# Optimization experiments

Hardware: AMD Instinct MI355X
Metric: run time of the kernel (lower is better)

The kernel has to match this reference:

```python
import jax, jax.numpy as jnp
import numpy as np

N, D = 2097152, 10  # tokens, feature dim (pinned by nn.Linear(10,10))


def setup_inputs() -> dict:
    key = jax.random.key(0)
    kx, kr, kw1, kb1, kw2, kb2 = jax.random.split(key, 6)
    s = 1.0 / np.sqrt(D)  # torch nn.Linear default init range
    x = jax.random.normal(kx, (N, D), dtype=jnp.float32)
    route = jax.random.randint(kr, (N,), 0, 2, dtype=jnp.int32)  # RandScatter decision
    W1 = jax.random.uniform(kw1, (D, D), jnp.float32, -s, s)
    b1 = jax.random.uniform(kb1, (D,), jnp.float32, -s, s)
    W2 = jax.random.uniform(kw2, (D, D), jnp.float32, -s, s)
    b2 = jax.random.uniform(kb2, (D,), jnp.float32, -s, s)
    return {"x": x, "W1": W1, "b1": b1, "W2": W2, "b2": b2, "route": route}


def reference(x, W1, b1, W2, b2, route):
    # Original: scatter rows by `route` to expert1/expert2 (Linear 10->10),
    # then gather back to original row order. Equivalent dense form:
    # out[i] = expert_{route[i]}(x[i]). The 10x10 GEMMs are negligible, so
    # computing both branches and selecting is the efficient vectorized form.
    y0 = x @ W1.T + b1  # [N, D] expert1 on all rows
    y1 = x @ W2.T + b2  # [N, D] expert2 on all rows
    return jnp.where((route == 0)[:, None], y0, y1)
```

## Files before the change

### kernel.cpp

```cpp
#include <hip/hip_runtime.h>


#define ROWS_PER_THREAD 4
#define BLOCK 256
#define D 10

__global__ __launch_bounds__(BLOCK) void moe_kernel(
    const float* __restrict__ x,
    const float* __restrict__ W1,
    const float* __restrict__ b1,
    const float* __restrict__ W2,
    const float* __restrict__ b2,
    const int*   __restrict__ route,
    float*       __restrict__ out,
    int n)
{
    const long long tid  = (long long)blockIdx.x * BLOCK + threadIdx.x;
    const long long row0 = tid * ROWS_PER_THREAD;
    if (row0 >= n) return;

    if (row0 + ROWS_PER_THREAD <= n) {
        const float4* __restrict__ xv = (const float4*)(x + row0 * D);
        float4*       __restrict__ ov = (float4*)(out + row0 * D);

        float v[ROWS_PER_THREAD * D];
        #pragma unroll
        for (int i = 0; i < 10; ++i) {
            float4 t = xv[i];
            v[i * 4 + 0] = t.x; v[i * 4 + 1] = t.y;
            v[i * 4 + 2] = t.z; v[i * 4 + 3] = t.w;
        }

        int4 rt = *(const int4*)(route + row0);
        int rsel[ROWS_PER_THREAD] = {rt.x, rt.y, rt.z, rt.w};

        #pragma unroll
        for (int r = 0; r < ROWS_PER_THREAD; ++r) {
            float y[D];
            #pragma unroll
            for (int j = 0; j < D; ++j) {
                float y0 = b1[j];
                float y1 = b2[j];
                #pragma unroll
                for (int k = 0; k < D; ++k) {
                    const float xk = v[r * D + k];
                    y0 = fmaf(xk, W1[j * D + k], y0);
                    y1 = fmaf(xk, W2[j * D + k], y1);
                }
                y[j] = (rsel[r] != 0) ? y1 : y0;
            }
            #pragma unroll
            for (int j = 0; j < D; ++j) v[r * D + j] = y[j];
        }

        #pragma unroll
        for (int i = 0; i < 10; ++i) {
            float4 t;
            t.x = v[i * 4 + 0]; t.y = v[i * 4 + 1];
            t.z = v[i * 4 + 2]; t.w = v[i * 4 + 3];
            ov[i] = t;
        }
    } else {
        for (long long row = row0; row < n; ++row) {
            const int sel = route[row];
            for (int j = 0; j < D; ++j) {
                float y0 = b1[j];
                float y1 = b2[j];
                for (int k = 0; k < D; ++k) {
                    const float xk = x[row * D + k];
                    y0 = fmaf(xk, W1[j * D + k], y0);
                    y1 = fmaf(xk, W2[j * D + k], y1);
                }
                out[row * D + j] = sel ? y1 : y0;
            }
        }
    }
}

extern "C" void kernel_launch(void* const* d_in, const int* in_sizes, int n_in,
                              void* d_out, int out_size, void* d_ws, size_t ws_size,
                              hipStream_t stream) {
    const float* x     = (const float*)d_in[0];
    const float* W1    = (const float*)d_in[1];
    const float* b1    = (const float*)d_in[2];
    const float* W2    = (const float*)d_in[3];
    const float* b2    = (const float*)d_in[4];
    const int*   route = (const int*)d_in[5];
    float*       out   = (float*)d_out;

    const int n = in_sizes[5];
    const int rows_per_block = BLOCK * ROWS_PER_THREAD;
    const int blocks = (n + rows_per_block - 1) / rows_per_block;

    moe_kernel<<<blocks, BLOCK, 0, stream>>>(x, W1, b1, W2, b2, route, out, n);
}
```

Before: 179.8 us.

## Stage rows through LDS per wave for fully coalesced global loads and stores

Each wave now loads a contiguous 128-row chunk of x with lane-strided float4 loads into shared memory, then each lane reads its own 2 rows back from LDS. Outputs are written into LDS and stored back with coalesced lane-strided float4 stores. Rows per thread drop from 4 to 2, which raises the thread count and lowers register pressure. The cost of the layout transpose is extra LDS traffic, possible bank conflicts from the stride-5 float4 access, and wave-level barriers.

```diff
diff --git a/kernel.cpp b/kernel.cpp
--- a/kernel.cpp
+++ b/kernel.cpp
@@ -1,9 +1,11 @@
 #include <hip/hip_runtime.h>
 
 
-#define ROWS_PER_THREAD 4
 #define BLOCK 256
 #define D 10
+#define ROWS_PER_WAVE 128
+#define ROWS_PER_BLOCK 512
+#define F4_PER_WAVE 320
 
 __global__ __launch_bounds__(BLOCK) void moe_kernel(
     const float* __restrict__ x,
@@ -15,63 +17,85 @@
     float*       __restrict__ out,
     int n)
 {
-    const long long tid  = (long long)blockIdx.x * BLOCK + threadIdx.x;
-    const long long row0 = tid * ROWS_PER_THREAD;
-    if (row0 >= n) return;
+    __shared__ float4 lds[(BLOCK / 64) * F4_PER_WAVE];
 
-    if (row0 + ROWS_PER_THREAD <= n) {
-        const float4* __restrict__ xv = (const float4*)(x + row0 * D);
-        float4*       __restrict__ ov = (float4*)(out + row0 * D);
+    const int lane = threadIdx.x & 63;
+    const int wave = threadIdx.x >> 6;
+    const long long rowbase =
+        ((long long)blockIdx.x * (BLOCK / 64) + wave) * ROWS_PER_WAVE;
 
-        float v[ROWS_PER_THREAD * D];
+    float4* __restrict__ wlds = lds + wave * F4_PER_WAVE;
+
+    if (rowbase + ROWS_PER_WAVE <= n) {
+        const float4* __restrict__ xv = (const float4*)(x + rowbase * D);
+        float4*       __restrict__ ov = (float4*)(out + rowbase * D);
+
         #pragma unroll
-        for (int i = 0; i < 10; ++i) {
-            float4 t = xv[i];
-            v[i * 4 + 0] = t.x; v[i * 4 + 1] = t.y;
-            v[i * 4 + 2] = t.z; v[i * 4 + 3] = t.w;
+        for (int j = 0; j < 5; ++j)
+            wlds[j * 64 + lane] = xv[j * 64 + lane];
+
+        const int2 rt = ((const int2*)(route + rowbase))[lane];
+        const int rsel[2] = {rt.x, rt.y};
+
+        __builtin_amdgcn_wave_barrier();
+
+        float4 xr[5];
+        #pragma unroll
+        for (int j = 0; j < 5; ++j)
+            xr[j] = wlds[lane * 5 + j];
+
+        float xf[2 * D];
+        #pragma unroll
+        for (int j = 0; j < 5; ++j) {
+            xf[4 * j + 0] = xr[j].x; xf[4 * j + 1] = xr[j].y;
+            xf[4 * j + 2] = xr[j].z; xf[4 * j + 3] = xr[j].w;
         }
 
-        int4 rt = *(const int4*)(route + row0);
-        int rsel[ROWS_PER_THREAD] = {rt.x, rt.y, rt.z, rt.w};
-
+        float yf[2 * D];
         #pragma unroll
-        for (int r = 0; r < ROWS_PER_THREAD; ++r) {
-            float y[D];
+        for (int r = 0; r < 2; ++r) {
             #pragma unroll
             for (int j = 0; j < D; ++j) {
                 float y0 = b1[j];
                 float y1 = b2[j];
                 #pragma unroll
                 for (int k = 0; k < D; ++k) {
-                    const float xk = v[r * D + k];
+                    const float xk = xf[r * D + k];
                     y0 = fmaf(xk, W1[j * D + k], y0);
                     y1 = fmaf(xk, W2[j * D + k], y1);
                 }
-                y[j] = (rsel[r] != 0) ? y1 : y0;
+                yf[r * D + j] = rsel[r] ? y1 : y0;
             }
-            #pragma unroll
-            for (int j = 0; j < D; ++j) v[r * D + j] = y[j];
         }
 
         #pragma unroll
-        for (int i = 0; i < 10; ++i) {
+        for (int j = 0; j < 5; ++j) {
             float4 t;
-            t.x = v[i * 4 + 0]; t.y = v[i * 4 + 1];
-            t.z = v[i * 4 + 2]; t.w = v[i * 4 + 3];
-            ov[i] = t;
+            t.x = yf[4 * j + 0]; t.y = yf[4 * j + 1];
+            t.z = yf[4 * j + 2]; t.w = yf[4 * j + 3];
+            wlds[lane * 5 + j] = t;
         }
+
+        __builtin_amdgcn_wave_barrier();
+
+        #pragma unroll
+        for (int j = 0; j < 5; ++j)
+            ov[j * 64 + lane] = wlds[j * 64 + lane];
     } else {
-        for (long long row = row0; row < n; ++row) {
-            const int sel = route[row];
-            for (int j = 0; j < D; ++j) {
-                float y0 = b1[j];
-                float y1 = b2[j];
-                for (int k = 0; k < D; ++k) {
-                    const float xk = x[row * D + k];
-                    y0 = fmaf(xk, W1[j * D + k], y0);
-                    y1 = fmaf(xk, W2[j * D + k], y1);
+        for (int r = 0; r < 2; ++r) {
+            const long long row = rowbase + lane * 2 + r;
+            if (row < n) {
+                const int sel = route[row];
+                for (int j = 0; j < D; ++j) {
+                    float y0 = b1[j];
+                    float y1 = b2[j];
+                    for (int k = 0; k < D; ++k) {
+                        const float xk = x[row * D + k];
+                        y0 = fmaf(xk, W1[j * D + k], y0);
+                        y1 = fmaf(xk, W2[j * D + k], y1);
+                    }
+                    out[row * D + j] = sel ? y1 : y0;
                 }
-                out[row * D + j] = sel ? y1 : y0;
             }
         }
     }
@@ -89,8 +113,7 @@
     float*       out   = (float*)d_out;
 
     const int n = in_sizes[5];
-    const int rows_per_block = BLOCK * ROWS_PER_THREAD;
-    const int blocks = (n + rows_per_block - 1) / rows_per_block;
+    const int blocks = (n + ROWS_PER_BLOCK - 1) / ROWS_PER_BLOCK;
 
     moe_kernel<<<blocks, BLOCK, 0, stream>>>(x, W1, b1, W2, b2, route, out, n);
 }
```

Result: faster. 165.5 us (-8.0%).
